# Kernel optimization log

Measured on AMD Instinct MI355X. Metric: run time of the kernel, lower is better.

## Reference

```python
import jax, jax.numpy as jnp
import numpy as np

N = 50000      # nodes
E = 800000     # edges
D = 256        # hidden_dim (input node features)
A = 128        # attention_dim = attention_ratio * heads
H = 8          # heads
DK = A // H    # 16


def setup_inputs() -> dict:
    key = jax.random.key(0)
    ks = jax.random.split(key, 6)
    x = jax.random.normal(ks[0], (N, D), dtype=jnp.float32)
    # small weight scale keeps exp(pre) well-conditioned (module uses tiny const init)
    Wq = jax.random.normal(ks[1], (A, D), dtype=jnp.float32) * 0.02
    bq = jnp.full((A,), 0.01, dtype=jnp.float32)
    Wk = jax.random.normal(ks[2], (A, D), dtype=jnp.float32) * 0.02
    bk = jnp.full((A,), 0.01, dtype=jnp.float32)
    edge_index = jax.random.randint(ks[3], (2, E), 0, N, dtype=jnp.int32)
    # d0_index[1] holds the two node indices each duplicated edge score scatters to
    d0_index = jax.random.randint(ks[4], (2, 2 * E), 0, N, dtype=jnp.int32)
    return {"x": x, "Wq": Wq, "bq": bq, "Wk": Wk, "bk": bk,
            "edge_index": edge_index, "d0_index": d0_index}


def reference(x, Wq, bq, Wk, bk, edge_index, d0_index):
    # linear projections -> [N, H, DK]
    q = (x @ Wq.T + bq).reshape(N, H, DK)
    k = (x @ Wk.T + bk).reshape(N, H, DK)
    src, dst = edge_index[0], edge_index[1]
    q_i = q[src]   # [E, H, DK]
    k_j = k[dst]
    q_j = q[dst]
    k_i = k[src]
    # symmetrized scaled-dot attention score per edge/head
    pre = 0.5 * jnp.sum(q_i * k_j + q_j * k_i, axis=-1)  # [E, H]
    pre = jnp.mean(pre, axis=-1)                          # [E]
    diagA1 = jnp.exp(pre)
    # duplicate each edge score: (a, a, b, b, ...) == torch (view(-1,1)*ones(E,2)).view(-1)
    edge_score_per_node = jnp.repeat(diagA1, 2)           # [2E]
    diagA0 = jax.ops.segment_sum(edge_score_per_node, d0_index[1], num_segments=N)
    return diagA0, diagA1
```

## Files before the change

### kernel.cpp

```cpp
#include <hip/hip_runtime.h>
#include <hip/hip_bf16.h>

#define N_NODES 50000
#define N_EDGES 800000
#define DIM 256
#define QKDIM 256
#define NB_T  391
#define CAP   8192
#define ITEMS (2 * N_EDGES)
#define IPB   4096

typedef __bf16 bfrag  __attribute__((ext_vector_type(8)));
typedef __bf16 bf4    __attribute__((ext_vector_type(4)));
typedef float  ffrag  __attribute__((ext_vector_type(4)));
typedef float  f2     __attribute__((ext_vector_type(2)));
typedef float  f4v    __attribute__((ext_vector_type(4)));

#define EP_PITCH 272

__global__ __launch_bounds__(256) void prep_bin(
    const float* __restrict__ Wq, const float* __restrict__ Wk,
    __bf16* __restrict__ Wb,
    const int* __restrict__ d0, unsigned int* __restrict__ rec,
    int* __restrict__ cur)
{
    __shared__ int lcnt[NB_T];
    __shared__ int lbase[NB_T];
    const int tid = threadIdx.x;
    const int gtid = blockIdx.x * 256 + tid;

    const int i4 = gtid * 4;
    if (i4 < 65536) {
        const float* s = (i4 < 32768) ? (Wq + i4) : (Wk + (i4 - 32768));
        const float4 v = *(const float4*)s;
        bf4 o;
        o[0] = (__bf16)v.x; o[1] = (__bf16)v.y; o[2] = (__bf16)v.z; o[3] = (__bf16)v.w;
        *(bf4*)(Wb + i4) = o;
    }

    for (int b = tid; b < NB_T; b += 256) lcnt[b] = 0;
    __syncthreads();
    const int base = blockIdx.x * IPB;
    int tg[16];
    #pragma unroll
    for (int r = 0; r < 16; ++r) {
        const int i = base + r * 256 + tid;
        tg[r] = (i < ITEMS) ? d0[i] : -1;
        if (tg[r] >= 0) atomicAdd(&lcnt[tg[r] >> 7], 1);
    }
    __syncthreads();

    for (int b = tid; b < NB_T; b += 256) {
        const int c = lcnt[b];
        lbase[b] = c ? atomicAdd(&cur[b], c) : 0;
    }
    __syncthreads();
    for (int b = tid; b < NB_T; b += 256) lcnt[b] = 0;
    __syncthreads();

    #pragma unroll
    for (int r = 0; r < 16; ++r) {
        if (tg[r] >= 0) {
            const int i = base + r * 256 + tid;
            const int b = tg[r] >> 7;
            const int off = atomicAdd(&lcnt[b], 1);
            rec[(size_t)b * CAP + lbase[b] + off] =
                ((unsigned int)(tg[r] & 127) << 20) | (unsigned int)(i >> 1);
        }
    }
}

__global__ __launch_bounds__(256) void proj_mfma(
    const float* __restrict__ x,
    const __bf16* __restrict__ Wb,
    const float* __restrict__ bq, const float* __restrict__ bk,
    unsigned char* __restrict__ qk8)
{
    __shared__ __bf16 As[64 * 256];

    const int tid  = threadIdx.x;
    const int wv   = tid >> 6;
    const int lane = tid & 63;
    const int m    = lane & 15;
    const int q    = lane >> 4;
    const int mbase = blockIdx.x * 64;

    {
        const int srow = tid >> 2;
        const int c4   = tid & 3;
        int grow = mbase + srow;
        grow = grow < N_NODES ? grow : N_NODES - 1;
        const float* xp = x + (size_t)grow * DIM;
        const int mt_ = srow >> 4, m_ = srow & 15;
        #pragma unroll
        for (int i = 0; i < 16; ++i) {
            const int k = c4 * 4 + 16 * i;
            const f4v v = __builtin_nontemporal_load((const f4v*)(xp + k));
            bf4 o;
            o[0] = (__bf16)v[0]; o[1] = (__bf16)v[1];
            o[2] = (__bf16)v[2]; o[3] = (__bf16)v[3];
            const int seg = (k >> 5) * 4 + mt_;
            const int ln  = ((k >> 3) & 3) * 16 + m_;
            *(bf4*)(As + seg * 512 + ln * 8 + (k & 7)) = o;
        }
    }
    __syncthreads();

    ffrag acc[4][4] = {};

    #pragma unroll
    for (int h = 0; h < 2; ++h) {
        bfrag b[4][4];
        #pragma unroll
        for (int sp = 0; sp < 4; ++sp)
            #pragma unroll
            for (int nt = 0; nt < 4; ++nt) {
                const int col = wv * 64 + nt * 16 + m;
                b[sp][nt] = *(const bfrag*)(Wb + (size_t)col * DIM
                                            + 32 * (4 * h + sp) + 8 * q);
            }
        #pragma unroll
        for (int sp = 0; sp < 4; ++sp) {
            bfrag a[4];
            #pragma unroll
            for (int mt = 0; mt < 4; ++mt)
                a[mt] = *(const bfrag*)(As + ((4 * h + sp) * 4 + mt) * 512 + lane * 8);
            #pragma unroll
            for (int mt = 0; mt < 4; ++mt)
                #pragma unroll
                for (int nt = 0; nt < 4; ++nt)
                    acc[mt][nt] = __builtin_amdgcn_mfma_f32_16x16x32_bf16(
                                      a[mt], b[sp][nt], acc[mt][nt], 0, 0, 0);
        }
    }

    __syncthreads();
    unsigned char* ep = (unsigned char*)As;
    #pragma unroll
    for (int nt = 0; nt < 4; ++nt) {
        const int col  = wv * 64 + nt * 16 + m;
        const float bias = (col < 128) ? bq[col] : bk[col - 128];
        #pragma unroll
        for (int mt = 0; mt < 4; ++mt) {
            #pragma unroll
            for (int r = 0; r < 4; ++r) {
                const int rl = mt * 16 + q * 4 + r;
                const float v = acc[mt][nt][r] + bias;
                const int pk = __builtin_amdgcn_cvt_pk_fp8_f32(v, v, 0, false);
                ep[rl * EP_PITCH + col] = (unsigned char)(pk & 0xFF);
            }
        }
    }
    __syncthreads();
    {
        const int rl = tid >> 2;
        const int ch = tid & 3;
        const int grow = mbase + rl;
        if (grow < N_NODES) {
            const uint4* s4 = (const uint4*)(ep + rl * EP_PITCH + ch * 64);
            const uint4 t0 = s4[0], t1 = s4[1], t2 = s4[2], t3 = s4[3];
            uint4* g = (uint4*)(qk8 + (size_t)grow * QKDIM + ch * 64);
            g[0] = t0; g[1] = t1; g[2] = t2; g[3] = t3;
        }
    }
}

__global__ __launch_bounds__(256) void edge_compute(
    const unsigned char* __restrict__ qk8,
    const int* __restrict__ edge_index,
    float* __restrict__ out)
{
    const int wave = (blockIdx.x * blockDim.x + threadIdx.x) >> 6;
    const int lane = threadIdx.x & 63;
    const int g = lane >> 2;
    const int j = lane & 3;
    const int e = wave * 16 + g;

    const int src = __builtin_nontemporal_load(edge_index + e);
    const int dst = __builtin_nontemporal_load(edge_index + N_EDGES + e);

    const uint4* rs = (const uint4*)(qk8 + (size_t)src * QKDIM + 64 * j);
    const uint4* rd = (const uint4*)(qk8 + (size_t)dst * QKDIM + 64 * ((j + 2) & 3));

    uint4 a[4], b[4];
    #pragma unroll
    for (int i = 0; i < 4; ++i) { a[i] = rs[i]; b[i] = rd[i]; }

    f2 acc = {0.f, 0.f};
    #pragma unroll
    for (int i = 0; i < 4; ++i) {
        const unsigned int* ua = (const unsigned int*)&a[i];
        const unsigned int* ub = (const unsigned int*)&b[i];
        #pragma unroll
        for (int t = 0; t < 4; ++t) {
            const f2 x0 = __builtin_amdgcn_cvt_pk_f32_fp8(ua[t], false);
            const f2 y0 = __builtin_amdgcn_cvt_pk_f32_fp8(ub[t], false);
            const f2 x1 = __builtin_amdgcn_cvt_pk_f32_fp8(ua[t], true);
            const f2 y1 = __builtin_amdgcn_cvt_pk_f32_fp8(ub[t], true);
            acc += x0 * y0;
            acc += x1 * y1;
        }
    }
    float p = acc[0] + acc[1];

    p += __shfl_xor(p, 1, 64);
    p += __shfl_xor(p, 2, 64);

    if (j == 0)
        out[N_NODES + e] = __expf(p * 0.0625f);
}

__global__ __launch_bounds__(1024) void phase_scatter(
    const unsigned int* __restrict__ rec, const int* __restrict__ cur,
    float* __restrict__ out)
{
    __shared__ float acc[128];
    const int b = blockIdx.x;
    const int tid = threadIdx.x;
    if (tid < 128) acc[tid] = 0.f;
    __syncthreads();

    const int cnt = cur[b];
    const unsigned int* rb = rec + (size_t)b * CAP;
    for (int i = tid; i < cnt; i += 1024) {
        const unsigned int r = rb[i];
        const float v = out[N_NODES + (r & 0xFFFFF)];
        atomicAdd(&acc[r >> 20], v);
    }
    __syncthreads();

    if (tid < 128) {
        const int n = b * 128 + tid;
        if (n < N_NODES) out[n] = acc[tid];
    }
}

extern "C" void kernel_launch(void* const* d_in, const int* in_sizes, int n_in,
                              void* d_out, int out_size, void* d_ws, size_t ws_size,
                              hipStream_t stream) {
    const float* x  = (const float*)d_in[0];
    const float* Wq = (const float*)d_in[1];
    const float* bq = (const float*)d_in[2];
    const float* Wk = (const float*)d_in[3];
    const float* bk = (const float*)d_in[4];
    const int* edge_index = (const int*)d_in[5];
    const int* d0 = (const int*)d_in[6] + 2 * N_EDGES;
    float* out = (float*)d_out;

    char* w = (char*)d_ws;
    unsigned char* qk8 = (unsigned char*)w;  w += (size_t)N_NODES * QKDIM;
    __bf16* Wb = (__bf16*)w;                 w += 131072;
    unsigned int* rec = (unsigned int*)w;    w += (size_t)NB_T * CAP * 4;
    int* cur = (int*)w;                      w += 2048;

    hipMemsetAsync(cur, 0, NB_T * sizeof(int), stream);
    prep_bin<<<NB_T, 256, 0, stream>>>(Wq, Wk, Wb, d0, rec, cur);
    proj_mfma<<<(N_NODES + 63) / 64, 256, 0, stream>>>(x, Wb, bq, bk, qk8);
    edge_compute<<<N_EDGES / 64, 256, 0, stream>>>(qk8, edge_index, out);
    phase_scatter<<<NB_T, 1024, 0, stream>>>(rec, cur, out);
}
```

Before: 207.5 us.

## Bin edges by source-node bucket so the edge kernel gathers with better locality

The prep kernel gains a second counting-sort pass that groups edges by source-node bucket of 128 nodes. It packs src, dst and the edge id into a 64-bit record per edge. The edge kernel then walks these bucketed records, so source-row gathers from the fp8 Q/K table hit a small working set and should reuse cache better. This costs an extra pass over edge_index, about 6 MB of record writes and reads, and a larger workspace; it falls back to the old direct kernel if the workspace is too small. The per-bucket capacity for the scatter records is also reduced.

Result: slower. 219.1 us (+5.6%).

```diff
diff --git a/kernel.cpp b/kernel.cpp
--- a/kernel.cpp
+++ b/kernel.cpp
@@ -6,9 +6,12 @@
 #define DIM 256
 #define QKDIM 256
 #define NB_T  391
-#define CAP   8192
+#define CAP   6144
+#define CAP2  2816
+#define BPB2  44
 #define ITEMS (2 * N_EDGES)
 #define IPB   4096
+#define EPB2  2048
 
 typedef __bf16 bfrag  __attribute__((ext_vector_type(8)));
 typedef __bf16 bf4    __attribute__((ext_vector_type(4)));
@@ -22,7 +25,9 @@
     const float* __restrict__ Wq, const float* __restrict__ Wk,
     __bf16* __restrict__ Wb,
     const int* __restrict__ d0, unsigned int* __restrict__ rec,
-    int* __restrict__ cur)
+    int* __restrict__ cur,
+    const int* __restrict__ edge_index, uint2* __restrict__ rec2,
+    int* __restrict__ cur2, int do_edges)
 {
     __shared__ int lcnt[NB_T];
     __shared__ int lbase[NB_T];
@@ -49,7 +54,6 @@
         if (tg[r] >= 0) atomicAdd(&lcnt[tg[r] >> 7], 1);
     }
     __syncthreads();
-
     for (int b = tid; b < NB_T; b += 256) {
         const int c = lcnt[b];
         lbase[b] = c ? atomicAdd(&cur[b], c) : 0;
@@ -57,7 +61,6 @@
     __syncthreads();
     for (int b = tid; b < NB_T; b += 256) lcnt[b] = 0;
     __syncthreads();
-
     #pragma unroll
     for (int r = 0; r < 16; ++r) {
         if (tg[r] >= 0) {
@@ -66,6 +69,42 @@
             const int off = atomicAdd(&lcnt[b], 1);
             rec[(size_t)b * CAP + lbase[b] + off] =
                 ((unsigned int)(tg[r] & 127) << 20) | (unsigned int)(i >> 1);
+        }
+    }
+
+    if (!do_edges) return;
+
+    __syncthreads();
+    for (int b = tid; b < NB_T; b += 256) lcnt[b] = 0;
+    __syncthreads();
+    const int ebase = blockIdx.x * EPB2;
+    int es[8], ed[8];
+    #pragma unroll
+    for (int r = 0; r < 8; ++r) {
+        const int e = ebase + r * 256 + tid;
+        es[r] = (e < N_EDGES) ? edge_index[e] : -1;
+        ed[r] = (e < N_EDGES) ? edge_index[N_EDGES + e] : 0;
+        if (es[r] >= 0) atomicAdd(&lcnt[es[r] >> 7], 1);
+    }
+    __syncthreads();
+    for (int b = tid; b < NB_T; b += 256) {
+        const int c = lcnt[b];
+        lbase[b] = c ? atomicAdd(&cur2[b], c) : 0;
+    }
+    __syncthreads();
+    for (int b = tid; b < NB_T; b += 256) lcnt[b] = 0;
+    __syncthreads();
+    #pragma unroll
+    for (int r = 0; r < 8; ++r) {
+        if (es[r] >= 0) {
+            const int e = ebase + r * 256 + tid;
+            const int b = es[r] >> 7;
+            const int off = atomicAdd(&lcnt[b], 1);
+            const unsigned long long pk = (unsigned long long)(unsigned)es[r]
+                | ((unsigned long long)(unsigned)ed[r] << 17)
+                | ((unsigned long long)(unsigned)e << 34);
+            rec2[(size_t)b * CAP2 + lbase[b] + off] =
+                make_uint2((unsigned)pk, (unsigned)(pk >> 32));
         }
     }
 }
@@ -167,30 +206,36 @@
 
 __global__ __launch_bounds__(256) void edge_compute(
     const unsigned char* __restrict__ qk8,
-    const int* __restrict__ edge_index,
+    const uint2* __restrict__ rec2, const int* __restrict__ cur2,
     float* __restrict__ out)
 {
-    const int wave = (blockIdx.x * blockDim.x + threadIdx.x) >> 6;
+    const int b = blockIdx.x / BPB2;
+    const int c = blockIdx.x - b * BPB2;
     const int lane = threadIdx.x & 63;
     const int g = lane >> 2;
     const int j = lane & 3;
-    const int e = wave * 16 + g;
-
-    const int src = __builtin_nontemporal_load(edge_index + e);
-    const int dst = __builtin_nontemporal_load(edge_index + N_EDGES + e);
+    const int idx = c * 64 + ((threadIdx.x >> 6) << 4) + g;
+
+    if (idx >= cur2[b]) return;
+
+    const uint2 rw = rec2[(size_t)b * CAP2 + idx];
+    const unsigned long long pk = ((unsigned long long)rw.y << 32) | rw.x;
+    const int src = (int)(pk & 0x1FFFF);
+    const int dst = (int)((pk >> 17) & 0x1FFFF);
+    const int e   = (int)(pk >> 34);
 
     const uint4* rs = (const uint4*)(qk8 + (size_t)src * QKDIM + 64 * j);
     const uint4* rd = (const uint4*)(qk8 + (size_t)dst * QKDIM + 64 * ((j + 2) & 3));
 
-    uint4 a[4], b[4];
-    #pragma unroll
-    for (int i = 0; i < 4; ++i) { a[i] = rs[i]; b[i] = rd[i]; }
+    uint4 a[4], bb[4];
+    #pragma unroll
+    for (int i = 0; i < 4; ++i) { a[i] = rs[i]; bb[i] = rd[i]; }
 
     f2 acc = {0.f, 0.f};
     #pragma unroll
     for (int i = 0; i < 4; ++i) {
         const unsigned int* ua = (const unsigned int*)&a[i];
-        const unsigned int* ub = (const unsigned int*)&b[i];
+        const unsigned int* ub = (const unsigned int*)&bb[i];
         #pragma unroll
         for (int t = 0; t < 4; ++t) {
             const f2 x0 = __builtin_amdgcn_cvt_pk_f32_fp8(ua[t], false);
@@ -202,7 +247,49 @@
         }
     }
     float p = acc[0] + acc[1];
-
+    p += __shfl_xor(p, 1, 64);
+    p += __shfl_xor(p, 2, 64);
+
+    if (j == 0)
+        out[N_NODES + e] = __expf(p * 0.0625f);
+}
+
+__global__ __launch_bounds__(256) void edge_direct(
+    const unsigned char* __restrict__ qk8,
+    const int* __restrict__ edge_index,
+    float* __restrict__ out)
+{
+    const int wave = (blockIdx.x * blockDim.x + threadIdx.x) >> 6;
+    const int lane = threadIdx.x & 63;
+    const int g = lane >> 2, j = lane & 3;
+    const int e = wave * 16 + g;
+
+    const int src = __builtin_nontemporal_load(edge_index + e);
+    const int dst = __builtin_nontemporal_load(edge_index + N_EDGES + e);
+
+    const uint4* rs = (const uint4*)(qk8 + (size_t)src * QKDIM + 64 * j);
+    const uint4* rd = (const uint4*)(qk8 + (size_t)dst * QKDIM + 64 * ((j + 2) & 3));
+
+    uint4 a[4], b[4];
+    #pragma unroll
+    for (int i = 0; i < 4; ++i) { a[i] = rs[i]; b[i] = rd[i]; }
+
+    f2 acc = {0.f, 0.f};
+    #pragma unroll
+    for (int i = 0; i < 4; ++i) {
+        const unsigned int* ua = (const unsigned int*)&a[i];
+        const unsigned int* ub = (const unsigned int*)&b[i];
+        #pragma unroll
+        for (int t = 0; t < 4; ++t) {
+            const f2 x0 = __builtin_amdgcn_cvt_pk_f32_fp8(ua[t], false);
+            const f2 y0 = __builtin_amdgcn_cvt_pk_f32_fp8(ub[t], false);
+            const f2 x1 = __builtin_amdgcn_cvt_pk_f32_fp8(ua[t], true);
+            const f2 y1 = __builtin_amdgcn_cvt_pk_f32_fp8(ub[t], true);
+            acc += x0 * y0;
+            acc += x1 * y1;
+        }
+    }
+    float p = acc[0] + acc[1];
     p += __shfl_xor(p, 1, 64);
     p += __shfl_xor(p, 2, 64);
 
@@ -251,11 +338,20 @@
     unsigned char* qk8 = (unsigned char*)w;  w += (size_t)N_NODES * QKDIM;
     __bf16* Wb = (__bf16*)w;                 w += 131072;
     unsigned int* rec = (unsigned int*)w;    w += (size_t)NB_T * CAP * 4;
-    int* cur = (int*)w;                      w += 2048;
-
-    hipMemsetAsync(cur, 0, NB_T * sizeof(int), stream);
-    prep_bin<<<NB_T, 256, 0, stream>>>(Wq, Wk, Wb, d0, rec, cur);
+    uint2* rec2 = (uint2*)w;                 w += (size_t)NB_T * CAP2 * 8;
+    int* cur = (int*)w;                      w += 4096;
+
+    const size_t need = (size_t)(w - (char*)d_ws);
+    const int use_sorted = (ws_size >= need) ? 1 : 0;
+    int* cur2 = cur + NB_T;
+
+    hipMemsetAsync(cur, 0, 2 * NB_T * sizeof(int), stream);
+    prep_bin<<<NB_T, 256, 0, stream>>>(Wq, Wk, Wb, d0, rec, cur,
+                                       edge_index, rec2, cur2, use_sorted);
     proj_mfma<<<(N_NODES + 63) / 64, 256, 0, stream>>>(x, Wb, bq, bk, qk8);
-    edge_compute<<<N_EDGES / 64, 256, 0, stream>>>(qk8, edge_index, out);
+    if (use_sorted)
+        edge_compute<<<NB_T * BPB2, 256, 0, stream>>>(qk8, rec2, cur2, out);
+    else
+        edge_direct<<<N_EDGES / 64, 256, 0, stream>>>(qk8, edge_index, out);
     phase_scatter<<<NB_T, 1024, 0, stream>>>(rec, cur, out);
 }
```
